# Optimization experiments

Hardware: AMD Instinct MI355X
Metric: run time of the kernel (lower is better)

Reference implementation:

```python
import jax, jax.numpy as jnp
import numpy as np

N = 16384
MUL0, MUL1, MUL2 = 128, 64, 32            # multiplicities of 0e, 1e, 2e
A = 16                                    # node_attr_dim (Ax0e)
D0, D1, D2 = MUL0, MUL1 * 3, MUL2 * 5     # e3nn flat block sizes
DIN = D0 + D1 + D2                        # 480
NGATE = MUL1 + MUL2                       # 96 gate scalars
OUT0 = MUL0 + NGATE                       # 224 scalar (0e) outputs of fctp_1


def setup_inputs() -> dict:
    key = jax.random.key(0)
    ks = jax.random.split(key, 10)
    f32 = jnp.float32
    return {
        "node_vec": jax.random.normal(ks[0], (N, DIN), f32),
        "node_embedding": jax.random.normal(ks[1], (N, A), f32),
        # fctp_1 path weights (fully-connected TP with Ax0e attr)
        "W1_l0": jax.random.normal(ks[2], (MUL0, A, OUT0), f32),
        "W1_l1": jax.random.normal(ks[3], (MUL1, A, MUL1), f32),
        "W1_l2": jax.random.normal(ks[4], (MUL2, A, MUL2), f32),
        "b1": jnp.zeros((OUT0,), f32),
        # fctp_2 scalar-path weight (only 0e x 0e -> 0e path exists)
        "W2": jax.random.normal(ks[5], (MUL0, A, A), f32),
        "b2": jnp.zeros((A,), f32),
        # scalar readout MLP: LinearRS -> SiLU -> LinearRS
        "W3": jax.random.normal(ks[6], (A, A), f32),
        "b3": jnp.zeros((A,), f32),
        "W4": jax.random.normal(ks[7], (A, 1), f32),
        "b4": jnp.zeros((1,), f32),
    }


def reference(node_vec, node_embedding, W1_l0, W1_l1, W1_l2, b1, W2, b2, W3, b3, W4, b4):
    # split e3nn-layout features into per-l blocks [N, mul, 2l+1]
    x0 = node_vec[:, :D0]                               # [N, 128]   l=0
    x1 = node_vec[:, D0:D0 + D1].reshape(-1, MUL1, 3)   # [N, 64, 3] l=1
    x2 = node_vec[:, D0 + D1:].reshape(-1, MUL2, 5)     # [N, 32, 5] l=2
    a = node_embedding                                  # [N, A] 0e scalars
    # fctp_1: fully-connected TP with Ax0e attr -> per-l bilinear mix (path-normalized)
    s = jnp.einsum('ni,na,iak->nk', x0, a, W1_l0) / np.sqrt(MUL0 * A) + b1  # [N, 224]
    y1 = jnp.einsum('nim,na,iak->nkm', x1, a, W1_l1) / np.sqrt(MUL1 * A)    # [N, 64, 3]
    y2 = jnp.einsum('nim,na,iak->nkm', x2, a, W1_l2) / np.sqrt(MUL2 * A)    # [N, 32, 5]
    # SwishGate: SiLU on scalars, sigmoid gates multiply the l>0 channels
    scalars = jax.nn.silu(s[:, :MUL0])
    gates = jax.nn.sigmoid(s[:, MUL0:])
    y1 = y1 * gates[:, :MUL1, None]
    y2 = y2 * gates[:, MUL1:, None]
    # fctp_2: output irreps = Ax0e, so only the 0e x 0e -> 0e path exists;
    # the gated l>0 features have no path to 0e (same as the torch TP).
    mid = jnp.einsum('ni,na,iak->nk', scalars, a, W2) / np.sqrt(MUL0 * A) + b2  # [N, A]
    # output_network: LinearRS -> SiLU -> LinearRS (rescale 1/sqrt(fan_in))
    h = jax.nn.silu(mid @ W3 / np.sqrt(A) + b3)
    return h @ W4 / np.sqrt(A) + b4                     # [N, 1]
```

## Files before the change

### kernel.cpp

```cpp
#include <hip/hip_runtime.h>


#define NKC 64

typedef _Float16 h8 __attribute__((ext_vector_type(8)));
typedef _Float16 h2 __attribute__((ext_vector_type(2)));
typedef float    f32x4 __attribute__((ext_vector_type(4)));
typedef unsigned int u32;

static __device__ __forceinline__ u32 pack2h(float a, float b) {
    h2 t = {(_Float16)a, (_Float16)b};
    return __builtin_bit_cast(u32, t);
}
static __device__ __forceinline__ f32x4 mfma_h(uint4 a, uint4 b, f32x4 c) {
    return __builtin_amdgcn_mfma_f32_16x16x32_f16(
        __builtin_bit_cast(h8, a), __builtin_bit_cast(h8, b), c, 0, 0, 0);
}
static __device__ __forceinline__ uint4 mk_afrag(_Float16 xh, const h2* ee) {
    h2 xx = {xh, xh};
    uint4 r;
    r.x = __builtin_bit_cast(u32, (h2)(xx * ee[0]));
    r.y = __builtin_bit_cast(u32, (h2)(xx * ee[1]));
    r.z = __builtin_bit_cast(u32, (h2)(xx * ee[2]));
    r.w = __builtin_bit_cast(u32, (h2)(xx * ee[3]));
    return r;
}
static __device__ __forceinline__ void async16(const void* g, void* l) {
    __builtin_amdgcn_global_load_lds(
        (const __attribute__((address_space(1))) u32*)g,
        (__attribute__((address_space(3))) u32*)l, 16, 0, 0);
}

__global__ __launch_bounds__(256) void prep_kernel(
        const float* __restrict__ W1, const float* __restrict__ W2,
        _Float16* __restrict__ W1T, _Float16* __restrict__ W2T) {
    const int b = blockIdx.x, kc = b >> 2, tp = b & 3;
    const int tid = threadIdx.x;
    __shared__ float l1[32 * 36];
    __shared__ float l2[32 * 20];

    {
        int row = tid >> 3, c4 = tid & 7;
        float4 v = *(const float4*)(W1 + (size_t)(kc * 32 + row) * 224 + tp * 32 + c4 * 4);
        *(float4*)(l1 + row * 36 + c4 * 4) = v;
    }
    if (tp == 0 && tid < 128) {
        int row = tid >> 2, c4 = tid & 3;
        float4 v = *(const float4*)(W2 + (size_t)(kc * 32 + row) * 16 + c4 * 4);
        *(float4*)(l2 + row * 20 + c4 * 4) = v;
    }
    __syncthreads();

    if (tid < 128) {
        int tl = tid >> 6, t = tp * 2 + tl, lane = tid & 63;
        int q = lane >> 4, cc = lane & 15, colL = tl * 16 + cc;
        u32 w[4];
#pragma unroll
        for (int jj = 0; jj < 4; ++jj)
            w[jj] = pack2h(l1[(q * 8 + 2 * jj) * 36 + colL],
                           l1[(q * 8 + 2 * jj + 1) * 36 + colL]);
        *(uint4*)(W1T + (size_t)kc * 4096 + (t * 64 + lane) * 8) =
            make_uint4(w[0], w[1], w[2], w[3]);
    }
    if (tp == 0 && tid >= 128 && tid < 192) {
        int lane = tid - 128, q = lane >> 4, cc = lane & 15;
        u32 w[4];
#pragma unroll
        for (int jj = 0; jj < 4; ++jj)
            w[jj] = pack2h(l2[(q * 8 + 2 * jj) * 20 + cc],
                           l2[(q * 8 + 2 * jj + 1) * 20 + cc]);
        *(uint4*)(W2T + (size_t)kc * 512 + lane * 8) = make_uint4(w[0], w[1], w[2], w[3]);
    }
}

__global__ __launch_bounds__(1024, 4) void main_kernel(
        const float* __restrict__ node_vec, const float* __restrict__ emb,
        const _Float16* __restrict__ W1T, const _Float16* __restrict__ W2T,
        const float* __restrict__ b1, const float* __restrict__ b2,
        const float* __restrict__ W3, const float* __restrict__ b3,
        const float* __restrict__ W4, const float* __restrict__ b4,
        float* __restrict__ out) {
    __shared__ __align__(16) char smem[52368];
    char*     ldsB = smem;
    _Float16* xe   = (_Float16*)(smem + 32768);
    _Float16* xo   = (_Float16*)(smem + 41984);
    float*    midp = (float*)smem;
    float*    mids = (float*)(smem + 17408);
    float*    w3s  = (float*)(smem + 51200);
    float*    b3s  = (float*)(smem + 52224);
    float*    w4s  = (float*)(smem + 52288);
    float*    b4s  = (float*)(smem + 52352);

    const int tid  = threadIdx.x;
    const int wave = tid >> 6, lane = tid & 63;
    const int q = lane >> 4, c = lane & 15;
    const int ih = q >> 1;
    const int aodd = q & 1;
    const int g  = wave >> 2;
    const int cq = wave & 3;
    const int nodeBase = blockIdx.x * 64;

    for (int idx = tid; idx < 2048; idx += 1024) {
        int row = idx >> 5, c4 = idx & 31;
        float4 v = *(const float4*)(node_vec + (size_t)(nodeBase + row) * 480 + c4 * 4);
        h2 ev = {(_Float16)v.x, (_Float16)v.z};
        h2 ov = {(_Float16)v.y, (_Float16)v.w};
        *(h2*)(xe + row * 72 + c4 * 2) = ev;
        *(h2*)(xo + row * 72 + c4 * 2) = ov;
    }
    if (tid < 256) w3s[tid] = W3[tid];
    if (tid < 16) { b3s[tid] = b3[tid]; w4s[tid] = W4[tid]; }
    if (tid == 0) b4s[0] = b4[0];

    h2 ee[4];
    {
        const float* ep = emb + (size_t)(nodeBase + g * 16 + c) * 16 + aodd * 8;
        float4 v0 = *(const float4*)ep;
        float4 v1 = *(const float4*)(ep + 4);
        ee[0] = (h2){(_Float16)v0.x, (_Float16)v0.y};
        ee[1] = (h2){(_Float16)v0.z, (_Float16)v0.w};
        ee[2] = (h2){(_Float16)v1.x, (_Float16)v1.y};
        ee[3] = (h2){(_Float16)v1.z, (_Float16)v1.w};
    }

    f32x4 acc0 = (f32x4){0.f, 0.f, 0.f, 0.f};
    f32x4 acc1 = (f32x4){0.f, 0.f, 0.f, 0.f};

    const int klw = wave >> 3, tw = wave & 7;
    const char* srcBase = (const char*)W1T + (size_t)((klw * 8 + tw) * 1024) + lane * 16;
    char* dstBase = ldsB + wave * 1024;

    const _Float16* xrow = (ih ? xo : xe) + (g * 16 + c) * 72;
    const int fo0 = (cq * 2) * 1024 + lane * 16;
    const int fo1 = (cq * 2 + 1) * 1024 + lane * 16;

    async16(srcBase, dstBase);
    __syncthreads();

    for (int ch = 0; ch < 32; ++ch) {
        if (ch + 1 < 32)
            async16(srcBase + (size_t)(ch + 1) * 16384, dstBase + ((ch + 1) & 1) * 16384);
        const char* buf = ldsB + (ch & 1) * 16384;
        h2 xx = *(const h2*)(xrow + 2 * ch);
#pragma unroll
        for (int kl = 0; kl < 2; ++kl) {
            uint4 f0 = *(const uint4*)(buf + kl * 8192 + fo0);
            uint4 f1 = *(const uint4*)(buf + kl * 8192 + fo1);
            uint4 af = mk_afrag(xx[kl], ee);
            acc0 = mfma_h(af, f0, acc0);
            acc1 = mfma_h(af, f1, acc1);
        }
        __syncthreads();
    }

    const float inv2048 = 0.022097086912079608f;
#pragma unroll
    for (int tt = 0; tt < 2; ++tt) {
        int t = cq * 2 + tt;
        float bb1v = b1[t * 16 + c];
        const f32x4& av = tt ? acc1 : acc0;
        _Float16* dst = (c & 1) ? xo : xe;
        int colh = t * 8 + (c >> 1);
#pragma unroll
        for (int r = 0; r < 4; ++r) {
            int node = g * 16 + q * 4 + r;
            float s  = av[r] * inv2048 + bb1v;
            float sc = s / (1.f + __expf(-s));
            dst[node * 72 + colh] = (_Float16)sc;
        }
    }
    __syncthreads();

    {
        const int ks = cq;
        const _Float16* srow = (ih ? xo : xe) + (g * 16 + c) * 72 + ks * 16;
        h8 sx0 = *(const h8*)(srow);
        h8 sx1 = *(const h8*)(srow + 8);
        const uint4* b2p = (const uint4*)W2T + lane;
        f32x4 macc = (f32x4){0.f, 0.f, 0.f, 0.f};
        uint4 wb[4];
#pragma unroll
        for (int u = 0; u < 4; ++u) wb[u] = b2p[(ks * 16 + u) * 64];
#pragma unroll
        for (int k2 = 0; k2 < 16; ++k2) {
            uint4 cur = wb[k2 & 3];
            if (k2 + 4 < 16) wb[k2 & 3] = b2p[(ks * 16 + k2 + 4) * 64];
            _Float16 sv = (k2 < 8) ? sx0[k2] : sx1[k2 - 8];
            macc = mfma_h(mk_afrag(sv, ee), cur, macc);
        }
#pragma unroll
        for (int r = 0; r < 4; ++r) {
            int node = g * 16 + q * 4 + r;
            midp[(ks * 64 + node) * 17 + c] = macc[r];
        }
    }
    __syncthreads();

    {
        int node = tid >> 4, col = tid & 15;
        float m = midp[node * 17 + col] + midp[(64 + node) * 17 + col]
                + midp[(128 + node) * 17 + col] + midp[(192 + node) * 17 + col];
        mids[node * 17 + col] = m * inv2048 + b2[col];
    }
    __syncthreads();

    {
        int n = tid >> 4, jj = tid & 15;
        float a = 0.f;
#pragma unroll
        for (int cc = 0; cc < 16; ++cc) a += mids[n * 17 + cc] * w3s[cc * 16 + jj];
        a = a * 0.25f + b3s[jj];
        float hh = a / (1.f + __expf(-a));
        float po = hh * w4s[jj];
        po += __shfl_xor(po, 1);
        po += __shfl_xor(po, 2);
        po += __shfl_xor(po, 4);
        po += __shfl_xor(po, 8);
        if (jj == 0) out[nodeBase + n] = po * 0.25f + b4s[0];
    }
}

extern "C" void kernel_launch(void* const* d_in, const int* in_sizes, int n_in,
                              void* d_out, int out_size, void* d_ws, size_t ws_size,
                              hipStream_t stream) {
    const float* node_vec = (const float*)d_in[0];
    const float* emb      = (const float*)d_in[1];
    const float* W1       = (const float*)d_in[2];
    const float* b1v      = (const float*)d_in[5];
    const float* W2       = (const float*)d_in[6];
    const float* b2v      = (const float*)d_in[7];
    const float* W3       = (const float*)d_in[8];
    const float* b3v      = (const float*)d_in[9];
    const float* W4       = (const float*)d_in[10];
    const float* b4v      = (const float*)d_in[11];

    _Float16* W1T = (_Float16*)d_ws;
    _Float16* W2T = W1T + 64 * 4096;
    float* out = (float*)d_out;

    prep_kernel<<<256, 256, 0, stream>>>(W1, W2, W1T, W2T);
    main_kernel<<<256, 1024, 0, stream>>>(node_vec, emb, W1T, W2T,
                                          b1v, b2v, W3, b3v, W4, b4v, out);
}
```

Measured before the change: 115.2 us.

## Stream W1 fragments into registers and reuse each across four node groups

Drops the async global-to-LDS double-buffered W1 staging and its per-chunk barriers. Each of the 8 waves now owns one output column tile and loads its W1 fragments straight from global memory into an 8-deep register ring. Each fragment feeds four MFMAs, one per 16-node group, so B operands are reused instead of re-read from LDS. The block shrinks from 1024 to 512 threads, so each wave does more work and holds more registers. Global weight loads now sit on the critical path, with only 8 stages of prefetch to hide them.

```diff
diff --git a/kernel.cpp b/kernel.cpp
--- a/kernel.cpp
+++ b/kernel.cpp
@@ -25,11 +25,6 @@
     r.w = __builtin_bit_cast(u32, (h2)(xx * ee[3]));
     return r;
 }
-static __device__ __forceinline__ void async16(const void* g, void* l) {
-    __builtin_amdgcn_global_load_lds(
-        (const __attribute__((address_space(1))) u32*)g,
-        (__attribute__((address_space(3))) u32*)l, 16, 0, 0);
-}
 
 __global__ __launch_bounds__(256) void prep_kernel(
         const float* __restrict__ W1, const float* __restrict__ W2,
@@ -73,34 +68,30 @@
     }
 }
 
-__global__ __launch_bounds__(1024, 4) void main_kernel(
+__global__ __launch_bounds__(512, 2) void main_kernel(
         const float* __restrict__ node_vec, const float* __restrict__ emb,
         const _Float16* __restrict__ W1T, const _Float16* __restrict__ W2T,
         const float* __restrict__ b1, const float* __restrict__ b2,
         const float* __restrict__ W3, const float* __restrict__ b3,
         const float* __restrict__ W4, const float* __restrict__ b4,
         float* __restrict__ out) {
-    __shared__ __align__(16) char smem[52368];
-    char*     ldsB = smem;
-    _Float16* xe   = (_Float16*)(smem + 32768);
-    _Float16* xo   = (_Float16*)(smem + 41984);
-    float*    midp = (float*)smem;
-    float*    mids = (float*)(smem + 17408);
-    float*    w3s  = (float*)(smem + 51200);
-    float*    b3s  = (float*)(smem + 52224);
-    float*    w4s  = (float*)(smem + 52288);
-    float*    b4s  = (float*)(smem + 52352);
+    __shared__ _Float16 xe[64 * 72];
+    __shared__ _Float16 xo[64 * 72];
+    __shared__ float    midp[4 * 64 * 17];
+    __shared__ float    mids[64 * 17];
+    __shared__ float    w3s[256];
+    __shared__ float    b3s[16];
+    __shared__ float    w4s[16];
+    __shared__ float    b4s[1];
 
     const int tid  = threadIdx.x;
     const int wave = tid >> 6, lane = tid & 63;
     const int q = lane >> 4, c = lane & 15;
     const int ih = q >> 1;
     const int aodd = q & 1;
-    const int g  = wave >> 2;
-    const int cq = wave & 3;
     const int nodeBase = blockIdx.x * 64;
 
-    for (int idx = tid; idx < 2048; idx += 1024) {
+    for (int idx = tid; idx < 2048; idx += 512) {
         int row = idx >> 5, c4 = idx & 31;
         float4 v = *(const float4*)(node_vec + (size_t)(nodeBase + row) * 480 + c4 * 4);
         h2 ev = {(_Float16)v.x, (_Float16)v.z};
@@ -112,72 +103,85 @@
     if (tid < 16) { b3s[tid] = b3[tid]; w4s[tid] = W4[tid]; }
     if (tid == 0) b4s[0] = b4[0];
 
-    h2 ee[4];
-    {
+    h2 eeg[4][4];
+#pragma unroll
+    for (int g = 0; g < 4; ++g) {
         const float* ep = emb + (size_t)(nodeBase + g * 16 + c) * 16 + aodd * 8;
         float4 v0 = *(const float4*)ep;
         float4 v1 = *(const float4*)(ep + 4);
-        ee[0] = (h2){(_Float16)v0.x, (_Float16)v0.y};
-        ee[1] = (h2){(_Float16)v0.z, (_Float16)v0.w};
-        ee[2] = (h2){(_Float16)v1.x, (_Float16)v1.y};
-        ee[3] = (h2){(_Float16)v1.z, (_Float16)v1.w};
-    }
-
-    f32x4 acc0 = (f32x4){0.f, 0.f, 0.f, 0.f};
-    f32x4 acc1 = (f32x4){0.f, 0.f, 0.f, 0.f};
-
-    const int klw = wave >> 3, tw = wave & 7;
-    const char* srcBase = (const char*)W1T + (size_t)((klw * 8 + tw) * 1024) + lane * 16;
-    char* dstBase = ldsB + wave * 1024;
-
-    const _Float16* xrow = (ih ? xo : xe) + (g * 16 + c) * 72;
-    const int fo0 = (cq * 2) * 1024 + lane * 16;
-    const int fo1 = (cq * 2 + 1) * 1024 + lane * 16;
-
-    async16(srcBase, dstBase);
-    __syncthreads();
-
-    for (int ch = 0; ch < 32; ++ch) {
-        if (ch + 1 < 32)
-            async16(srcBase + (size_t)(ch + 1) * 16384, dstBase + ((ch + 1) & 1) * 16384);
-        const char* buf = ldsB + (ch & 1) * 16384;
-        h2 xx = *(const h2*)(xrow + 2 * ch);
-#pragma unroll
-        for (int kl = 0; kl < 2; ++kl) {
-            uint4 f0 = *(const uint4*)(buf + kl * 8192 + fo0);
-            uint4 f1 = *(const uint4*)(buf + kl * 8192 + fo1);
-            uint4 af = mk_afrag(xx[kl], ee);
-            acc0 = mfma_h(af, f0, acc0);
-            acc1 = mfma_h(af, f1, acc1);
-        }
-        __syncthreads();
-    }
+        eeg[g][0] = (h2){(_Float16)v0.x, (_Float16)v0.y};
+        eeg[g][1] = (h2){(_Float16)v0.z, (_Float16)v0.w};
+        eeg[g][2] = (h2){(_Float16)v1.x, (_Float16)v1.y};
+        eeg[g][3] = (h2){(_Float16)v1.z, (_Float16)v1.w};
+    }
+    __syncthreads();
+
+    f32x4 acc[4];
+#pragma unroll
+    for (int g = 0; g < 4; ++g) acc[g] = (f32x4){0.f, 0.f, 0.f, 0.f};
+
+    const int t = wave;
+    const uint4* bp = (const uint4*)W1T + t * 64 + lane;
+    const _Float16* xbase = (ih ? xo : xe);
+    const _Float16* xrow0 = xbase + (0 * 16 + c) * 72;
+    const _Float16* xrow1 = xbase + (1 * 16 + c) * 72;
+    const _Float16* xrow2 = xbase + (2 * 16 + c) * 72;
+    const _Float16* xrow3 = xbase + (3 * 16 + c) * 72;
+
+    uint4 ring[8];
+#pragma unroll
+    for (int r = 0; r < 8; ++r) ring[r] = bp[r * 512];
+    h2 xh2[4];
+    xh2[0] = *(const h2*)xrow0; xh2[1] = *(const h2*)xrow1;
+    xh2[2] = *(const h2*)xrow2; xh2[3] = *(const h2*)xrow3;
+
+#pragma unroll 8
+    for (int kc = 0; kc < NKC; ++kc) {
+        uint4 cur = ring[kc & 7];
+        if (kc + 8 < NKC) ring[kc & 7] = bp[(kc + 8) * 512];
+        _Float16 xv0 = xh2[0][kc & 1], xv1 = xh2[1][kc & 1];
+        _Float16 xv2 = xh2[2][kc & 1], xv3 = xh2[3][kc & 1];
+        if ((kc & 1) && kc + 1 < NKC) {
+            int nx = kc + 1;
+            xh2[0] = *(const h2*)(xrow0 + nx); xh2[1] = *(const h2*)(xrow1 + nx);
+            xh2[2] = *(const h2*)(xrow2 + nx); xh2[3] = *(const h2*)(xrow3 + nx);
+        }
+        acc[0] = mfma_h(mk_afrag(xv0, eeg[0]), cur, acc[0]);
+        acc[1] = mfma_h(mk_afrag(xv1, eeg[1]), cur, acc[1]);
+        acc[2] = mfma_h(mk_afrag(xv2, eeg[2]), cur, acc[2]);
+        acc[3] = mfma_h(mk_afrag(xv3, eeg[3]), cur, acc[3]);
+    }
+
+    __syncthreads();
 
     const float inv2048 = 0.022097086912079608f;
-#pragma unroll
-    for (int tt = 0; tt < 2; ++tt) {
-        int t = cq * 2 + tt;
+    {
         float bb1v = b1[t * 16 + c];
-        const f32x4& av = tt ? acc1 : acc0;
         _Float16* dst = (c & 1) ? xo : xe;
         int colh = t * 8 + (c >> 1);
 #pragma unroll
-        for (int r = 0; r < 4; ++r) {
-            int node = g * 16 + q * 4 + r;
-            float s  = av[r] * inv2048 + bb1v;
-            float sc = s / (1.f + __expf(-s));
-            dst[node * 72 + colh] = (_Float16)sc;
-        }
-    }
-    __syncthreads();
-
-    {
-        const int ks = cq;
-        const _Float16* srow = (ih ? xo : xe) + (g * 16 + c) * 72 + ks * 16;
-        h8 sx0 = *(const h8*)(srow);
-        h8 sx1 = *(const h8*)(srow + 8);
+        for (int g = 0; g < 4; ++g) {
+#pragma unroll
+            for (int r = 0; r < 4; ++r) {
+                int node = g * 16 + q * 4 + r;
+                float s  = acc[g][r] * inv2048 + bb1v;
+                float sc = s / (1.f + __expf(-s));
+                dst[node * 72 + colh] = (_Float16)sc;
+            }
+        }
+    }
+    __syncthreads();
+
+    {
+        const int nh = wave >> 2, ks = wave & 3;
+        const _Float16* sbase = (ih ? xo : xe);
+        const _Float16* srow0 = sbase + ((nh * 2 + 0) * 16 + c) * 72 + ks * 16;
+        const _Float16* srow1 = sbase + ((nh * 2 + 1) * 16 + c) * 72 + ks * 16;
+        h8 s0a = *(const h8*)srow0, s0b = *(const h8*)(srow0 + 8);
+        h8 s1a = *(const h8*)srow1, s1b = *(const h8*)(srow1 + 8);
         const uint4* b2p = (const uint4*)W2T + lane;
-        f32x4 macc = (f32x4){0.f, 0.f, 0.f, 0.f};
+        f32x4 m0 = (f32x4){0.f, 0.f, 0.f, 0.f};
+        f32x4 m1 = (f32x4){0.f, 0.f, 0.f, 0.f};
         uint4 wb[4];
 #pragma unroll
         for (int u = 0; u < 4; ++u) wb[u] = b2p[(ks * 16 + u) * 64];
@@ -185,38 +189,50 @@
         for (int k2 = 0; k2 < 16; ++k2) {
             uint4 cur = wb[k2 & 3];
             if (k2 + 4 < 16) wb[k2 & 3] = b2p[(ks * 16 + k2 + 4) * 64];
-            _Float16 sv = (k2 < 8) ? sx0[k2] : sx1[k2 - 8];
-            macc = mfma_h(mk_afrag(sv, ee), cur, macc);
+            _Float16 sv0 = (k2 < 8) ? s0a[k2] : s0b[k2 - 8];
+            _Float16 sv1 = (k2 < 8) ? s1a[k2] : s1b[k2 - 8];
+            m0 = mfma_h(mk_afrag(sv0, eeg[nh * 2 + 0]), cur, m0);
+            m1 = mfma_h(mk_afrag(sv1, eeg[nh * 2 + 1]), cur, m1);
         }
 #pragma unroll
         for (int r = 0; r < 4; ++r) {
-            int node = g * 16 + q * 4 + r;
-            midp[(ks * 64 + node) * 17 + c] = macc[r];
-        }
-    }
-    __syncthreads();
-
-    {
-        int node = tid >> 4, col = tid & 15;
-        float m = midp[node * 17 + col] + midp[(64 + node) * 17 + col]
-                + midp[(128 + node) * 17 + col] + midp[(192 + node) * 17 + col];
-        mids[node * 17 + col] = m * inv2048 + b2[col];
-    }
-    __syncthreads();
-
-    {
-        int n = tid >> 4, jj = tid & 15;
-        float a = 0.f;
-#pragma unroll
-        for (int cc = 0; cc < 16; ++cc) a += mids[n * 17 + cc] * w3s[cc * 16 + jj];
-        a = a * 0.25f + b3s[jj];
-        float hh = a / (1.f + __expf(-a));
-        float po = hh * w4s[jj];
-        po += __shfl_xor(po, 1);
-        po += __shfl_xor(po, 2);
-        po += __shfl_xor(po, 4);
-        po += __shfl_xor(po, 8);
-        if (jj == 0) out[nodeBase + n] = po * 0.25f + b4s[0];
+            int n0 = (nh * 2 + 0) * 16 + q * 4 + r;
+            int n1 = (nh * 2 + 1) * 16 + q * 4 + r;
+            midp[(ks * 64 + n0) * 17 + c] = m0[r];
+            midp[(ks * 64 + n1) * 17 + c] = m1[r];
+        }
+    }
+    __syncthreads();
+
+    {
+        int n0 = tid >> 4, col = tid & 15;
+#pragma unroll
+        for (int half = 0; half < 2; ++half) {
+            int node = n0 + half * 32;
+            float m = midp[node * 17 + col] + midp[(64 + node) * 17 + col]
+                    + midp[(128 + node) * 17 + col] + midp[(192 + node) * 17 + col];
+            mids[node * 17 + col] = m * inv2048 + b2[col];
+        }
+    }
+    __syncthreads();
+
+    {
+        int n0 = tid >> 4, jj = tid & 15;
+#pragma unroll
+        for (int half = 0; half < 2; ++half) {
+            int n = n0 + half * 32;
+            float a = 0.f;
+#pragma unroll
+            for (int cc = 0; cc < 16; ++cc) a += mids[n * 17 + cc] * w3s[cc * 16 + jj];
+            a = a * 0.25f + b3s[jj];
+            float hh = a / (1.f + __expf(-a));
+            float po = hh * w4s[jj];
+            po += __shfl_xor(po, 1);
+            po += __shfl_xor(po, 2);
+            po += __shfl_xor(po, 4);
+            po += __shfl_xor(po, 8);
+            if (jj == 0) out[nodeBase + n] = po * 0.25f + b4s[0];
+        }
     }
 }
 
@@ -239,6 +255,6 @@
     float* out = (float*)d_out;
 
     prep_kernel<<<256, 256, 0, stream>>>(W1, W2, W1T, W2T);
-    main_kernel<<<256, 1024, 0, stream>>>(node_vec, emb, W1T, W2T,
-                                          b1v, b2v, W3, b3v, W4, b4v, out);
-}
+    main_kernel<<<256, 512, 0, stream>>>(node_vec, emb, W1T, W2T,
+                                         b1v, b2v, W3, b3v, W4, b4v, out);
+}
```

After: 113.2 us. Within noise of the previous version (-1.8%).
